# Kernel optimization log

Hardware: AMD Instinct MI355X
Metric: run time of the kernel (lower is better)

Reference implementation:

```python
import jax, jax.numpy as jnp
import numpy as np

B, T, N, H, P = 16, 64, 512, 128, 12


def _laplacian_with_self_loop(adj):
    a = adj + jnp.eye(adj.shape[0], dtype=adj.dtype)
    d_inv_sqrt = 1.0 / jnp.sqrt(a.sum(axis=1))
    return a * d_inv_sqrt[:, None] * d_inv_sqrt[None, :]


def setup_inputs() -> dict:
    key = jax.random.key(0)
    ks = jax.random.split(key, 10)
    inputs = jax.random.normal(ks[0], (B, T, N), dtype=jnp.float32)
    adj = jax.random.uniform(ks[1], (N, N), dtype=jnp.float32)
    adj = (adj + adj.T) * 0.5
    laplacian = _laplacian_with_self_loop(adj)

    def xavier(k, shape):
        fan_in, fan_out = shape[0], shape[1]
        lim = np.sqrt(6.0 / (fan_in + fan_out))
        return jax.random.uniform(k, shape, jnp.float32, -lim, lim)

    W1 = xavier(ks[2], (H + 1, 2 * H))      # graph_conv1 weights
    b1 = jnp.ones((2 * H,), jnp.float32)    # bias init 1.0
    W2 = xavier(ks[3], (H + 1, H))          # graph_conv2 weights
    b2 = jnp.zeros((H,), jnp.float32)
    att_w1 = xavier(ks[4], (H, 1))
    att_w2 = xavier(ks[5], (N, 1))
    att_w3 = xavier(ks[6], (N, 1))
    att_b1 = jnp.zeros((1,), jnp.float32)
    att_b2 = jnp.zeros((1,), jnp.float32)
    att_b3 = jnp.zeros((1,), jnp.float32)
    W_out = xavier(ks[7], (T, P))
    b_out = jnp.zeros((P,), jnp.float32)
    return dict(inputs=inputs, laplacian=laplacian, W1=W1, b1=b1, W2=W2, b2=b2,
                att_w1=att_w1, att_w2=att_w2, att_w3=att_w3,
                att_b1=att_b1, att_b2=att_b2, att_b3=att_b3,
                W_out=W_out, b_out=b_out)


def reference(inputs, laplacian, W1, b1, W2, b2,
              att_w1, att_w2, att_w3, att_b1, att_b2, att_b3,
              W_out, b_out):
    Bs, Ts, Ns = inputs.shape
    Hs = W2.shape[1]

    def graph_conv(x_t, h_flat, W, b):
        # x_t: [B,N]; h_flat: [B, N*H]
        h = h_flat.reshape(Bs, Ns, Hs)
        conc = jnp.concatenate([x_t[..., None], h], axis=-1)     # [B,N,H+1]
        agg = jnp.einsum('mn,bnc->bmc', laplacian, conc)          # [B,N,H+1]
        out = agg @ W + b                                         # [B,N,O]
        return out.reshape(Bs, -1)                                # [B,N*O] (flattened, matching torch)

    def step(h_flat, x_t):
        ru = jax.nn.sigmoid(graph_conv(x_t, h_flat, W1, b1))      # [B, N*2H]
        r, u = jnp.split(ru, 2, axis=1)                            # split on flattened dim (faithful)
        c = jnp.tanh(graph_conv(x_t, r * h_flat, W2, b2))          # [B, N*H]
        new_h = u * h_flat + (1.0 - u) * c
        return new_h, new_h

    h0 = jnp.zeros((Bs, Ns * Hs), inputs.dtype)
    _, hs = jax.lax.scan(step, h0, jnp.moveaxis(inputs, 1, 0))     # [T,B,N*H]
    hidden_states = jnp.moveaxis(hs, 0, 1).reshape(Bs, Ts, Ns, Hs)

    # SelfAttention: project H->1, then N->1 per (b,t), softmax over T
    hs1 = hidden_states.reshape(-1, Hs) @ att_w1 + att_b1          # [B*T*N, 1]
    f = (hs1.reshape(-1, Ns) @ att_w2 + att_b2).reshape(Bs, Ts)
    g = (hs1.reshape(-1, Ns) @ att_w3 + att_b3).reshape(Bs, Ts)
    beta = jax.nn.softmax(g * f, axis=-1)                          # [B,T]
    context = beta[:, :, None] * hs1.reshape(Bs, Ts, Ns)           # [B,T,N]

    context = context.transpose(0, 2, 1)                           # [B,N,T]
    Ps = W_out.shape[1]
    out = (context.reshape(-1, Ts) @ W_out + b_out).reshape(Bs, Ns, Ps)
    return out.transpose(0, 2, 1)                                  # [B,pre_len,N]
```

## Files before the change

kernel.cpp:

```cpp
#include <hip/hip_runtime.h>
#include <math.h>

#define B_ 16
#define T_ 64
#define N_ 512
#define H_ 128
#define P_ 12
#define NH 65536

__global__ __launch_bounds__(512) void lx_kernel(const float* __restrict__ x,
                                                 const float* __restrict__ L,
                                                 float* __restrict__ Lx) {
    __shared__ __align__(16) float xs[2][N_];
    const int r0 = blockIdx.x * 2;
    const int tid = threadIdx.x;
    for (int j = 0; j < 2; ++j)
        xs[j][tid] = x[(size_t)(r0 + j) * N_ + tid];
    __syncthreads();
    float a0 = 0.f, a1 = 0.f;
    const int m = tid;
#pragma unroll 8
    for (int n = 0; n < N_; ++n) {
        float lv = L[(size_t)n * N_ + m];
        a0 += xs[0][n] * lv;
        a1 += xs[1][n] * lv;
    }
    Lx[(size_t)(r0 + 0) * N_ + m] = a0;
    Lx[(size_t)(r0 + 1) * N_ + m] = a1;
}

#define FMA4(dst, a, hv)                                                      \
    dst[0] += (a) * (hv).x; dst[1] += (a) * (hv).y;                           \
    dst[2] += (a) * (hv).z; dst[3] += (a) * (hv).w;

__global__ __launch_bounds__(512) void gc1y_kernel(
    const float* __restrict__ L, const float* __restrict__ Hprev,
    const float* __restrict__ Lx, const float* __restrict__ W1,
    const float* __restrict__ b1, const float* __restrict__ W2,
    float* __restrict__ Y, float* __restrict__ u, int t) {
    __shared__ __align__(16) union Buf {
        float Ht[2][32][H_];
        struct { float R[32][132]; float Zb[16][132]; } s;
    } bb;
    __shared__ __align__(16) union LW {
        float Lt[2][32][20];
        float Wt[16][260];
    } sm;

    const int tid = threadIdx.x;
    const int b = blockIdx.x & 15;
    const int m0 = (blockIdx.x >> 4) * 16;
    const float* __restrict__ Hb = Hprev + (size_t)b * NH;

    const int hrow = tid >> 5, hcol = (tid & 31) * 4;
    const int lm = tid >> 5, lk = tid & 31;

    {
        *(float4*)&bb.Ht[0][hrow][hcol] =
            *(const float4*)&Hb[(size_t)hrow * H_ + hcol];
        *(float4*)&bb.Ht[0][hrow + 16][hcol] =
            *(const float4*)&Hb[(size_t)(hrow + 16) * H_ + hcol];
        sm.Lt[0][lk][lm] = L[(size_t)(m0 + lm) * N_ + lk];
    }
    __syncthreads();

    const int g = tid >> 6;
    const int l = tid & 63;
    const int ty = l >> 4;
    const int tx = l & 15;
    const int ma0 = ty * 4;
    const int ca0 = tx * 4, cb0 = 64 + tx * 4;

    float acc[4][2][4] = {};

    for (int kc = 0; kc < 16; ++kc) {
        const int bi = kc & 1, bj = bi ^ 1;
        float4 p0, p1;
        float pl;
        if (kc < 15) {
            const size_t kb = (size_t)(kc + 1) * 32;
            p0 = *(const float4*)&Hb[(kb + hrow) * H_ + hcol];
            p1 = *(const float4*)&Hb[(kb + hrow + 16) * H_ + hcol];
            pl = L[(size_t)(m0 + lm) * N_ + kb + lk];
        }
#pragma unroll
        for (int kk = 0; kk < 4; ++kk) {
            const int k = g * 4 + kk;
            const float4 la = *(const float4*)&sm.Lt[bi][k][ma0];
            const float4 h0 = *(const float4*)&bb.Ht[bi][k][ca0];
            const float4 h1 = *(const float4*)&bb.Ht[bi][k][cb0];
            FMA4(acc[0][0], la.x, h0) FMA4(acc[0][1], la.x, h1)
            FMA4(acc[1][0], la.y, h0) FMA4(acc[1][1], la.y, h1)
            FMA4(acc[2][0], la.z, h0) FMA4(acc[2][1], la.z, h1)
            FMA4(acc[3][0], la.w, h0) FMA4(acc[3][1], la.w, h1)
        }
        if (kc < 15) {
            *(float4*)&bb.Ht[bj][hrow][hcol] = p0;
            *(float4*)&bb.Ht[bj][hrow + 16][hcol] = p1;
            sm.Lt[bj][lk][lm] = pl;
        }
        __syncthreads();
    }

    for (int r = 0; r < 8; ++r) {
        if (g == r) {
#pragma unroll
            for (int i = 0; i < 4; ++i) {
#pragma unroll
                for (int v = 0; v < 2; ++v) {
                    const int c = v ? cb0 : ca0;
                    float4* zp = (float4*)&bb.s.Zb[ma0 + i][c];
                    if (r == 0) {
                        *zp = make_float4(acc[i][v][0], acc[i][v][1],
                                          acc[i][v][2], acc[i][v][3]);
                    } else {
                        float4 z = *zp;
                        *zp = make_float4(z.x + acc[i][v][0], z.y + acc[i][v][1],
                                          z.z + acc[i][v][2], z.w + acc[i][v][3]);
                    }
                }
            }
        }
        __syncthreads();
    }

    const int wv8 = tid >> 6;
    const int lr = l >> 3;
    const int lc = wv8 * 32 + (l & 7) * 4;
    float a2[2][4] = {};
    const int wr = tid >> 5, wc = (tid & 31) * 4;

#pragma unroll 1
    for (int ck = 0; ck < 8; ++ck) {
        *(float4*)&sm.Wt[wr][wc] =
            *(const float4*)&W1[(size_t)(1 + ck * 16 + wr) * 256 + wc];
        *(float4*)&sm.Wt[wr][wc + 128] =
            *(const float4*)&W1[(size_t)(1 + ck * 16 + wr) * 256 + wc + 128];
        __syncthreads();
#pragma unroll
        for (int ch4 = 0; ch4 < 4; ++ch4) {
            const int cc = ck * 16 + ch4 * 4;
            const float4 z0v = *(const float4*)&bb.s.Zb[lr][cc];
            const float4 z1v = *(const float4*)&bb.s.Zb[lr + 8][cc];
            const float4 w0v = *(const float4*)&sm.Wt[ch4 * 4 + 0][lc];
            const float4 w1v = *(const float4*)&sm.Wt[ch4 * 4 + 1][lc];
            const float4 w2v = *(const float4*)&sm.Wt[ch4 * 4 + 2][lc];
            const float4 w3v = *(const float4*)&sm.Wt[ch4 * 4 + 3][lc];
            a2[0][0] += z0v.x * w0v.x + z0v.y * w1v.x + z0v.z * w2v.x + z0v.w * w3v.x;
            a2[0][1] += z0v.x * w0v.y + z0v.y * w1v.y + z0v.z * w2v.y + z0v.w * w3v.y;
            a2[0][2] += z0v.x * w0v.z + z0v.y * w1v.z + z0v.z * w2v.z + z0v.w * w3v.z;
            a2[0][3] += z0v.x * w0v.w + z0v.y * w1v.w + z0v.z * w2v.w + z0v.w * w3v.w;
            a2[1][0] += z1v.x * w0v.x + z1v.y * w1v.x + z1v.z * w2v.x + z1v.w * w3v.x;
            a2[1][1] += z1v.x * w0v.y + z1v.y * w1v.y + z1v.z * w2v.y + z1v.w * w3v.y;
            a2[1][2] += z1v.x * w0v.z + z1v.y * w1v.z + z1v.z * w2v.z + z1v.w * w3v.z;
            a2[1][3] += z1v.x * w0v.w + z1v.y * w1v.w + z1v.z * w2v.w + z1v.w * w3v.w;
        }
        __syncthreads();
    }

    const float4 w0r = *(const float4*)&W1[lc];
    const float4 bbv = *(const float4*)&b1[lc];
    const float* __restrict__ LxRow = Lx + ((size_t)b * T_ + t) * N_ + m0;
    const bool isR = (m0 < 256);

    if (isR) {
#pragma unroll
        for (int i = 0; i < 2; ++i) {
            const int mi = lr + 8 * i;
            const float lx = LxRow[mi];
            float v0 = a2[i][0] + lx * w0r.x + bbv.x;
            float v1 = a2[i][1] + lx * w0r.y + bbv.y;
            float v2 = a2[i][2] + lx * w0r.z + bbv.z;
            float v3 = a2[i][3] + lx * w0r.w + bbv.w;
            float s0 = 1.f / (1.f + expf(-v0));
            float s1 = 1.f / (1.f + expf(-v1));
            float s2 = 1.f / (1.f + expf(-v2));
            float s3 = 1.f / (1.f + expf(-v3));
            const int fl = (m0 + mi) * 256 + lc;
            float4 hv = *(const float4*)&Hb[fl];
            *(float4*)&bb.s.R[2 * mi + (lc >> 7)][lc & 127] =
                make_float4(s0 * hv.x, s1 * hv.y, s2 * hv.z, s3 * hv.w);
        }
        __syncthreads();

        const int pr = l >> 2;
        const int pc = wv8 * 16 + (l & 3) * 4;
        float a3[2][4] = {};
#pragma unroll 1
        for (int ck = 0; ck < 8; ++ck) {
            *(float4*)&sm.Wt[wr][wc] =
                *(const float4*)&W2[(size_t)(1 + ck * 16 + wr) * H_ + wc];
            __syncthreads();
#pragma unroll
            for (int ch4 = 0; ch4 < 4; ++ch4) {
                const int cc = ck * 16 + ch4 * 4;
                const float4 z0v = *(const float4*)&bb.s.R[pr][cc];
                const float4 z1v = *(const float4*)&bb.s.R[pr + 16][cc];
                const float4 w0v = *(const float4*)&sm.Wt[ch4 * 4 + 0][pc];
                const float4 w1v = *(const float4*)&sm.Wt[ch4 * 4 + 1][pc];
                const float4 w2v = *(const float4*)&sm.Wt[ch4 * 4 + 2][pc];
                const float4 w3v = *(const float4*)&sm.Wt[ch4 * 4 + 3][pc];
                a3[0][0] += z0v.x * w0v.x + z0v.y * w1v.x + z0v.z * w2v.x + z0v.w * w3v.x;
                a3[0][1] += z0v.x * w0v.y + z0v.y * w1v.y + z0v.z * w2v.y + z0v.w * w3v.y;
                a3[0][2] += z0v.x * w0v.z + z0v.y * w1v.z + z0v.z * w2v.z + z0v.w * w3v.z;
                a3[0][3] += z0v.x * w0v.w + z0v.y * w1v.w + z0v.z * w2v.w + z0v.w * w3v.w;
                a3[1][0] += z1v.x * w0v.x + z1v.y * w1v.x + z1v.z * w2v.x + z1v.w * w3v.x;
                a3[1][1] += z1v.x * w0v.y + z1v.y * w1v.y + z1v.z * w2v.y + z1v.w * w3v.y;
                a3[1][2] += z1v.x * w0v.z + z1v.y * w1v.z + z1v.z * w2v.z + z1v.w * w3v.z;
                a3[1][3] += z1v.x * w0v.w + z1v.y * w1v.w + z1v.z * w2v.w + z1v.w * w3v.w;
            }
            __syncthreads();
        }
        float* __restrict__ Yb = Y + (size_t)b * NH;
        *(float4*)&Yb[(size_t)(2 * m0 + pr) * H_ + pc] =
            make_float4(a3[0][0], a3[0][1], a3[0][2], a3[0][3]);
        *(float4*)&Yb[(size_t)(2 * m0 + pr + 16) * H_ + pc] =
            make_float4(a3[1][0], a3[1][1], a3[1][2], a3[1][3]);
    } else {
        float* __restrict__ uB = u + (size_t)b * NH;
#pragma unroll
        for (int i = 0; i < 2; ++i) {
            const int mi = lr + 8 * i;
            const float lx = LxRow[mi];
            float v0 = a2[i][0] + lx * w0r.x + bbv.x;
            float v1 = a2[i][1] + lx * w0r.y + bbv.y;
            float v2 = a2[i][2] + lx * w0r.z + bbv.z;
            float v3 = a2[i][3] + lx * w0r.w + bbv.w;
            float s0 = 1.f / (1.f + expf(-v0));
            float s1 = 1.f / (1.f + expf(-v1));
            float s2 = 1.f / (1.f + expf(-v2));
            float s3 = 1.f / (1.f + expf(-v3));
            const int fl = (m0 + mi) * 256 + lc;
            *(float4*)&uB[fl - NH] = make_float4(s0, s1, s2, s3);
        }
    }
}

__global__ __launch_bounds__(512) void gcz_kernel(
    const float* __restrict__ L, const float* __restrict__ Y,
    const float* __restrict__ Hprev, const float* __restrict__ u,
    const float* __restrict__ Lx, const float* __restrict__ W2,
    const float* __restrict__ b2, const float* __restrict__ aw1,
    const float* __restrict__ ab1, float* __restrict__ Hnew,
    float* __restrict__ hs1, int t) {
    __shared__ __align__(16) union Buf {
        float Ht[2][32][H_];
        struct { float R[32][H_]; float Zb[16][H_]; } s;
    } bb;
    __shared__ __align__(16) float Lt[2][32][20];

    const int tid = threadIdx.x;
    const int b = blockIdx.x & 15;
    const int m0 = (blockIdx.x >> 4) * 16;
    const float* __restrict__ Yb = Y + (size_t)b * NH;

    const int hrow = tid >> 5, hcol = (tid & 31) * 4;
    const int lm = tid >> 5, lk = tid & 31;

    {
        *(float4*)&bb.Ht[0][hrow][hcol] =
            *(const float4*)&Yb[(size_t)hrow * H_ + hcol];
        *(float4*)&bb.Ht[0][hrow + 16][hcol] =
            *(const float4*)&Yb[(size_t)(hrow + 16) * H_ + hcol];
        Lt[0][lk][lm] = L[(size_t)(m0 + lm) * N_ + lk];
    }
    __syncthreads();

    const int g = tid >> 6;
    const int l = tid & 63;
    const int ty = l >> 4;
    const int tx = l & 15;
    const int ma0 = ty * 4;
    const int ca0 = tx * 4, cb0 = 64 + tx * 4;

    float acc[4][2][4] = {};

    for (int kc = 0; kc < 16; ++kc) {
        const int bi = kc & 1, bj = bi ^ 1;
        float4 p0, p1;
        float pl;
        if (kc < 15) {
            const size_t kb = (size_t)(kc + 1) * 32;
            p0 = *(const float4*)&Yb[(kb + hrow) * H_ + hcol];
            p1 = *(const float4*)&Yb[(kb + hrow + 16) * H_ + hcol];
            pl = L[(size_t)(m0 + lm) * N_ + kb + lk];
        }
#pragma unroll
        for (int kk = 0; kk < 4; ++kk) {
            const int k = g * 4 + kk;
            const float4 la = *(const float4*)&Lt[bi][k][ma0];
            const float4 h0 = *(const float4*)&bb.Ht[bi][k][ca0];
            const float4 h1 = *(const float4*)&bb.Ht[bi][k][cb0];
            FMA4(acc[0][0], la.x, h0) FMA4(acc[0][1], la.x, h1)
            FMA4(acc[1][0], la.y, h0) FMA4(acc[1][1], la.y, h1)
            FMA4(acc[2][0], la.z, h0) FMA4(acc[2][1], la.z, h1)
            FMA4(acc[3][0], la.w, h0) FMA4(acc[3][1], la.w, h1)
        }
        if (kc < 15) {
            *(float4*)&bb.Ht[bj][hrow][hcol] = p0;
            *(float4*)&bb.Ht[bj][hrow + 16][hcol] = p1;
            Lt[bj][lk][lm] = pl;
        }
        __syncthreads();
    }

    for (int r = 0; r < 8; ++r) {
        if (g == r) {
#pragma unroll
            for (int i = 0; i < 4; ++i) {
#pragma unroll
                for (int v = 0; v < 2; ++v) {
                    const int c = v ? cb0 : ca0;
                    float4* zp = (float4*)&bb.s.Zb[ma0 + i][c];
                    if (r == 0) {
                        *zp = make_float4(acc[i][v][0], acc[i][v][1],
                                          acc[i][v][2], acc[i][v][3]);
                    } else {
                        float4 z = *zp;
                        *zp = make_float4(z.x + acc[i][v][0], z.y + acc[i][v][1],
                                          z.z + acc[i][v][2], z.w + acc[i][v][3]);
                    }
                }
            }
        }
        __syncthreads();
    }

    const int zr = tid >> 5;
    const int zc = (tid & 31) * 4;
    const float4 zv = *(const float4*)&bb.s.Zb[zr][zc];
    const float4 w0r = *(const float4*)&W2[zc];
    const float4 bbv = *(const float4*)&b2[zc];
    const float4 awv = *(const float4*)&aw1[zc];
    const float lx = Lx[((size_t)b * T_ + t) * N_ + m0 + zr];

    float c0 = tanhf(zv.x + lx * w0r.x + bbv.x);
    float c1 = tanhf(zv.y + lx * w0r.y + bbv.y);
    float c2 = tanhf(zv.z + lx * w0r.z + bbv.z);
    float c3 = tanhf(zv.w + lx * w0r.w + bbv.w);

    const size_t fl = (size_t)b * NH + (size_t)(m0 + zr) * H_ + zc;
    const float4 uv = *(const float4*)&u[fl];
    const float4 hp = *(const float4*)&Hprev[fl];
    const float h0 = uv.x * hp.x + (1.f - uv.x) * c0;
    const float h1 = uv.y * hp.y + (1.f - uv.y) * c1;
    const float h2 = uv.z * hp.z + (1.f - uv.z) * c2;
    const float h3 = uv.w * hp.w + (1.f - uv.w) * c3;
    *(float4*)&Hnew[fl] = make_float4(h0, h1, h2, h3);

    float part = h0 * awv.x + h1 * awv.y + h2 * awv.z + h3 * awv.w;
#pragma unroll
    for (int off = 16; off; off >>= 1) part += __shfl_xor(part, off);
    if ((tid & 31) == 0)
        hs1[((size_t)b * T_ + t) * N_ + m0 + zr] = part + ab1[0];
}

__global__ __launch_bounds__(64) void att_beta_kernel(
    const float* __restrict__ hs1, const float* __restrict__ aw2,
    const float* __restrict__ aw3, const float* __restrict__ ab2,
    const float* __restrict__ ab3, float* __restrict__ beta) {
    const int b = blockIdx.x;
    const int t = threadIdx.x;
    const float* __restrict__ row = hs1 + ((size_t)b * T_ + t) * N_;
    float f = 0.f, g = 0.f;
    for (int n = 0; n < N_; n += 4) {
        float4 hv = *(const float4*)&row[n];
        float4 w2v = *(const float4*)&aw2[n];
        float4 w3v = *(const float4*)&aw3[n];
        f += hv.x * w2v.x + hv.y * w2v.y + hv.z * w2v.z + hv.w * w2v.w;
        g += hv.x * w3v.x + hv.y * w3v.y + hv.z * w3v.z + hv.w * w3v.w;
    }
    f += ab2[0];
    g += ab3[0];
    float s = f * g;
    float mx = s;
    for (int off = 32; off; off >>= 1) mx = fmaxf(mx, __shfl_xor(mx, off));
    float e = expf(s - mx);
    float sum = e;
    for (int off = 32; off; off >>= 1) sum += __shfl_xor(sum, off);
    beta[b * T_ + t] = e / sum;
}

__global__ __launch_bounds__(256) void att_out_kernel(
    const float* __restrict__ hs1, const float* __restrict__ beta,
    const float* __restrict__ Wout, const float* __restrict__ bout,
    float* __restrict__ out) {
    __shared__ float bs[T_];
    __shared__ float ws[T_][P_];
    const int b = blockIdx.x;
    const int tid = threadIdx.x;
    if (tid < T_) bs[tid] = beta[b * T_ + tid];
    for (int i = tid; i < T_ * P_; i += 256) ws[i / P_][i % P_] = Wout[i];
    __syncthreads();
    for (int nn = 0; nn < 2; ++nn) {
        const int n = tid + nn * 256;
        float acc[P_];
#pragma unroll
        for (int p = 0; p < P_; ++p) acc[p] = bout[p];
        for (int t = 0; t < T_; ++t) {
            float v = bs[t] * hs1[((size_t)b * T_ + t) * N_ + n];
#pragma unroll
            for (int p = 0; p < P_; ++p) acc[p] += v * ws[t][p];
        }
#pragma unroll
        for (int p = 0; p < P_; ++p) out[((size_t)b * P_ + p) * N_ + n] = acc[p];
    }
}

extern "C" void kernel_launch(void* const* d_in, const int* in_sizes, int n_in,
                              void* d_out, int out_size, void* d_ws, size_t ws_size,
                              hipStream_t stream) {
    const float* x = (const float*)d_in[0];
    const float* L = (const float*)d_in[1];
    const float* W1 = (const float*)d_in[2];
    const float* b1 = (const float*)d_in[3];
    const float* W2 = (const float*)d_in[4];
    const float* b2 = (const float*)d_in[5];
    const float* aw1 = (const float*)d_in[6];
    const float* aw2 = (const float*)d_in[7];
    const float* aw3 = (const float*)d_in[8];
    const float* ab1 = (const float*)d_in[9];
    const float* ab2 = (const float*)d_in[10];
    const float* ab3 = (const float*)d_in[11];
    const float* Wout = (const float*)d_in[12];
    const float* bout = (const float*)d_in[13];
    float* out = (float*)d_out;

    float* ws = (float*)d_ws;
    float* Lx = ws;
    float* hs1 = Lx + B_ * T_ * N_;
    float* hb0 = hs1 + B_ * T_ * N_;
    float* hb1 = hb0 + (size_t)B_ * NH;
    float* u = hb1 + (size_t)B_ * NH;
    float* Ybuf = u + (size_t)B_ * NH;
    float* beta = Ybuf + (size_t)B_ * NH;
    (void)in_sizes; (void)n_in; (void)out_size; (void)ws_size;

    hipMemsetAsync(hb0, 0, (size_t)B_ * NH * sizeof(float), stream);
    lx_kernel<<<512, 512, 0, stream>>>(x, L, Lx);

    for (int t = 0; t < T_; ++t) {
        float* hp = (t & 1) ? hb1 : hb0;
        float* hn = (t & 1) ? hb0 : hb1;
        gc1y_kernel<<<512, 512, 0, stream>>>(L, hp, Lx, W1, b1, W2, Ybuf, u, t);
        gcz_kernel<<<512, 512, 0, stream>>>(L, Ybuf, hp, u, Lx, W2, b2, aw1,
                                            ab1, hn, hs1, t);
    }
    att_beta_kernel<<<16, 64, 0, stream>>>(hs1, aw2, aw3, ab2, ab3, beta);
    att_out_kernel<<<16, 256, 0, stream>>>(hs1, beta, Wout, bout, out);
}
```

Baseline: 3.583 ms.

## Stage full L slice in LDS and read H and W directly from global

```diff
diff --git a/kernel.cpp b/kernel.cpp
--- a/kernel.cpp
+++ b/kernel.cpp
@@ -39,29 +39,20 @@
     const float* __restrict__ b1, const float* __restrict__ W2,
     float* __restrict__ Y, float* __restrict__ u, int t) {
     __shared__ __align__(16) union Buf {
-        float Ht[2][32][H_];
+        float Lt[512][20];
         struct { float R[32][132]; float Zb[16][132]; } s;
     } bb;
-    __shared__ __align__(16) union LW {
-        float Lt[2][32][20];
-        float Wt[16][260];
-    } sm;
 
     const int tid = threadIdx.x;
     const int b = blockIdx.x & 15;
     const int m0 = (blockIdx.x >> 4) * 16;
     const float* __restrict__ Hb = Hprev + (size_t)b * NH;
 
-    const int hrow = tid >> 5, hcol = (tid & 31) * 4;
     const int lm = tid >> 5, lk = tid & 31;
 
-    {
-        *(float4*)&bb.Ht[0][hrow][hcol] =
-            *(const float4*)&Hb[(size_t)hrow * H_ + hcol];
-        *(float4*)&bb.Ht[0][hrow + 16][hcol] =
-            *(const float4*)&Hb[(size_t)(hrow + 16) * H_ + hcol];
-        sm.Lt[0][lk][lm] = L[(size_t)(m0 + lm) * N_ + lk];
-    }
+#pragma unroll
+    for (int j = 0; j < 16; ++j)
+        bb.Lt[lk + 32 * j][lm] = L[(size_t)(m0 + lm) * N_ + lk + 32 * j];
     __syncthreads();
 
     const int g = tid >> 6;
@@ -72,35 +63,24 @@
     const int ca0 = tx * 4, cb0 = 64 + tx * 4;
 
     float acc[4][2][4] = {};
-
+    const float* __restrict__ h0p = Hb + ca0;
+    const float* __restrict__ h1p = Hb + cb0;
+
+#pragma unroll 1
     for (int kc = 0; kc < 16; ++kc) {
-        const int bi = kc & 1, bj = bi ^ 1;
-        float4 p0, p1;
-        float pl;
-        if (kc < 15) {
-            const size_t kb = (size_t)(kc + 1) * 32;
-            p0 = *(const float4*)&Hb[(kb + hrow) * H_ + hcol];
-            p1 = *(const float4*)&Hb[(kb + hrow + 16) * H_ + hcol];
-            pl = L[(size_t)(m0 + lm) * N_ + kb + lk];
-        }
 #pragma unroll
         for (int kk = 0; kk < 4; ++kk) {
-            const int k = g * 4 + kk;
-            const float4 la = *(const float4*)&sm.Lt[bi][k][ma0];
-            const float4 h0 = *(const float4*)&bb.Ht[bi][k][ca0];
-            const float4 h1 = *(const float4*)&bb.Ht[bi][k][cb0];
+            const int k = kc * 32 + g * 4 + kk;
+            const float4 la = *(const float4*)&bb.Lt[k][ma0];
+            const float4 h0 = *(const float4*)&h0p[(size_t)k * H_];
+            const float4 h1 = *(const float4*)&h1p[(size_t)k * H_];
             FMA4(acc[0][0], la.x, h0) FMA4(acc[0][1], la.x, h1)
             FMA4(acc[1][0], la.y, h0) FMA4(acc[1][1], la.y, h1)
             FMA4(acc[2][0], la.z, h0) FMA4(acc[2][1], la.z, h1)
             FMA4(acc[3][0], la.w, h0) FMA4(acc[3][1], la.w, h1)
         }
-        if (kc < 15) {
-            *(float4*)&bb.Ht[bj][hrow][hcol] = p0;
-            *(float4*)&bb.Ht[bj][hrow + 16][hcol] = p1;
-            sm.Lt[bj][lk][lm] = pl;
-        }
-        __syncthreads();
-    }
+    }
+    __syncthreads();
 
     for (int r = 0; r < 8; ++r) {
         if (g == r) {
@@ -128,24 +108,19 @@
     const int lr = l >> 3;
     const int lc = wv8 * 32 + (l & 7) * 4;
     float a2[2][4] = {};
-    const int wr = tid >> 5, wc = (tid & 31) * 4;
 
 #pragma unroll 1
     for (int ck = 0; ck < 8; ++ck) {
-        *(float4*)&sm.Wt[wr][wc] =
-            *(const float4*)&W1[(size_t)(1 + ck * 16 + wr) * 256 + wc];
-        *(float4*)&sm.Wt[wr][wc + 128] =
-            *(const float4*)&W1[(size_t)(1 + ck * 16 + wr) * 256 + wc + 128];
-        __syncthreads();
 #pragma unroll
         for (int ch4 = 0; ch4 < 4; ++ch4) {
             const int cc = ck * 16 + ch4 * 4;
             const float4 z0v = *(const float4*)&bb.s.Zb[lr][cc];
             const float4 z1v = *(const float4*)&bb.s.Zb[lr + 8][cc];
-            const float4 w0v = *(const float4*)&sm.Wt[ch4 * 4 + 0][lc];
-            const float4 w1v = *(const float4*)&sm.Wt[ch4 * 4 + 1][lc];
-            const float4 w2v = *(const float4*)&sm.Wt[ch4 * 4 + 2][lc];
-            const float4 w3v = *(const float4*)&sm.Wt[ch4 * 4 + 3][lc];
+            const int wrow = 1 + ck * 16 + ch4 * 4;
+            const float4 w0v = *(const float4*)&W1[(size_t)(wrow + 0) * 256 + lc];
+            const float4 w1v = *(const float4*)&W1[(size_t)(wrow + 1) * 256 + lc];
+            const float4 w2v = *(const float4*)&W1[(size_t)(wrow + 2) * 256 + lc];
+            const float4 w3v = *(const float4*)&W1[(size_t)(wrow + 3) * 256 + lc];
             a2[0][0] += z0v.x * w0v.x + z0v.y * w1v.x + z0v.z * w2v.x + z0v.w * w3v.x;
             a2[0][1] += z0v.x * w0v.y + z0v.y * w1v.y + z0v.z * w2v.y + z0v.w * w3v.y;
             a2[0][2] += z0v.x * w0v.z + z0v.y * w1v.z + z0v.z * w2v.z + z0v.w * w3v.z;
@@ -155,7 +130,6 @@
             a2[1][2] += z1v.x * w0v.z + z1v.y * w1v.z + z1v.z * w2v.z + z1v.w * w3v.z;
             a2[1][3] += z1v.x * w0v.w + z1v.y * w1v.w + z1v.z * w2v.w + z1v.w * w3v.w;
         }
-        __syncthreads();
     }
 
     const float4 w0r = *(const float4*)&W1[lc];
@@ -188,28 +162,25 @@
         float a3[2][4] = {};
 #pragma unroll 1
         for (int ck = 0; ck < 8; ++ck) {
-            *(float4*)&sm.Wt[wr][wc] =
-                *(const float4*)&W2[(size_t)(1 + ck * 16 + wr) * H_ + wc];
-            __syncthreads();
 #pragma unroll
             for (int ch4 = 0; ch4 < 4; ++ch4) {
                 const int cc = ck * 16 + ch4 * 4;
-                const float4 z0v = *(const float4*)&bb.s.R[pr][cc];
-                const float4 z1v = *(const float4*)&bb.s.R[pr + 16][cc];
-                const float4 w0v = *(const float4*)&sm.Wt[ch4 * 4 + 0][pc];
-                const float4 w1v = *(const float4*)&sm.Wt[ch4 * 4 + 1][pc];
-                const float4 w2v = *(const float4*)&sm.Wt[ch4 * 4 + 2][pc];
-                const float4 w3v = *(const float4*)&sm.Wt[ch4 * 4 + 3][pc];
-                a3[0][0] += z0v.x * w0v.x + z0v.y * w1v.x + z0v.z * w2v.x + z0v.w * w3v.x;
-                a3[0][1] += z0v.x * w0v.y + z0v.y * w1v.y + z0v.z * w2v.y + z0v.w * w3v.y;
-                a3[0][2] += z0v.x * w0v.z + z0v.y * w1v.z + z0v.z * w2v.z + z0v.w * w3v.z;
-                a3[0][3] += z0v.x * w0v.w + z0v.y * w1v.w + z0v.z * w2v.w + z0v.w * w3v.w;
-                a3[1][0] += z1v.x * w0v.x + z1v.y * w1v.x + z1v.z * w2v.x + z1v.w * w3v.x;
-                a3[1][1] += z1v.x * w0v.y + z1v.y * w1v.y + z1v.z * w2v.y + z1v.w * w3v.y;
-                a3[1][2] += z1v.x * w0v.z + z1v.y * w1v.z + z1v.z * w2v.z + z1v.w * w3v.z;
-                a3[1][3] += z1v.x * w0v.w + z1v.y * w1v.w + z1v.z * w2v.w + z1v.w * w3v.w;
+                const float4 z0 = *(const float4*)&bb.s.R[pr][cc];
+                const float4 z1 = *(const float4*)&bb.s.R[pr + 16][cc];
+                const int wrow = 1 + ck * 16 + ch4 * 4;
+                const float4 w0 = *(const float4*)&W2[(size_t)(wrow + 0) * H_ + pc];
+                const float4 w1 = *(const float4*)&W2[(size_t)(wrow + 1) * H_ + pc];
+                const float4 w2 = *(const float4*)&W2[(size_t)(wrow + 2) * H_ + pc];
+                const float4 w3 = *(const float4*)&W2[(size_t)(wrow + 3) * H_ + pc];
+                a3[0][0] += z0.x * w0.x + z0.y * w1.x + z0.z * w2.x + z0.w * w3.x;
+                a3[0][1] += z0.x * w0.y + z0.y * w1.y + z0.z * w2.y + z0.w * w3.y;
+                a3[0][2] += z0.x * w0.z + z0.y * w1.z + z0.z * w2.z + z0.w * w3.z;
+                a3[0][3] += z0.x * w0.w + z0.y * w1.w + z0.z * w2.w + z0.w * w3.w;
+                a3[1][0] += z1.x * w0.x + z1.y * w1.x + z1.z * w2.x + z1.w * w3.x;
+                a3[1][1] += z1.x * w0.y + z1.y * w1.y + z1.z * w2.y + z1.w * w3.y;
+                a3[1][2] += z1.x * w0.z + z1.y * w1.z + z1.z * w2.z + z1.w * w3.z;
+                a3[1][3] += z1.x * w0.w + z1.y * w1.w + z1.z * w2.w + z1.w * w3.w;
             }
-            __syncthreads();
         }
         float* __restrict__ Yb = Y + (size_t)b * NH;
         *(float4*)&Yb[(size_t)(2 * m0 + pr) * H_ + pc] =
@@ -244,26 +215,19 @@
     const float* __restrict__ ab1, float* __restrict__ Hnew,
     float* __restrict__ hs1, int t) {
     __shared__ __align__(16) union Buf {
-        float Ht[2][32][H_];
-        struct { float R[32][H_]; float Zb[16][H_]; } s;
+        float Lt[512][20];
+        float Zb[16][H_];
     } bb;
-    __shared__ __align__(16) float Lt[2][32][20];
 
     const int tid = threadIdx.x;
     const int b = blockIdx.x & 15;
     const int m0 = (blockIdx.x >> 4) * 16;
     const float* __restrict__ Yb = Y + (size_t)b * NH;
 
-    const int hrow = tid >> 5, hcol = (tid & 31) * 4;
     const int lm = tid >> 5, lk = tid & 31;
-
-    {
-        *(float4*)&bb.Ht[0][hrow][hcol] =
-            *(const float4*)&Yb[(size_t)hrow * H_ + hcol];
-        *(float4*)&bb.Ht[0][hrow + 16][hcol] =
-            *(const float4*)&Yb[(size_t)(hrow + 16) * H_ + hcol];
-        Lt[0][lk][lm] = L[(size_t)(m0 + lm) * N_ + lk];
-    }
+#pragma unroll
+    for (int j = 0; j < 16; ++j)
+        bb.Lt[lk + 32 * j][lm] = L[(size_t)(m0 + lm) * N_ + lk + 32 * j];
     __syncthreads();
 
     const int g = tid >> 6;
@@ -274,35 +238,24 @@
     const int ca0 = tx * 4, cb0 = 64 + tx * 4;
 
     float acc[4][2][4] = {};
-
+    const float* __restrict__ y0p = Yb + ca0;
+    const float* __restrict__ y1p = Yb + cb0;
+
+#pragma unroll 1
     for (int kc = 0; kc < 16; ++kc) {
-        const int bi = kc & 1, bj = bi ^ 1;
-        float4 p0, p1;
-        float pl;
-        if (kc < 15) {
-            const size_t kb = (size_t)(kc + 1) * 32;
-            p0 = *(const float4*)&Yb[(kb + hrow) * H_ + hcol];
-            p1 = *(const float4*)&Yb[(kb + hrow + 16) * H_ + hcol];
-            pl = L[(size_t)(m0 + lm) * N_ + kb + lk];
-        }
 #pragma unroll
         for (int kk = 0; kk < 4; ++kk) {
-            const int k = g * 4 + kk;
-            const float4 la = *(const float4*)&Lt[bi][k][ma0];
-            const float4 h0 = *(const float4*)&bb.Ht[bi][k][ca0];
-            const float4 h1 = *(const float4*)&bb.Ht[bi][k][cb0];
+            const int k = kc * 32 + g * 4 + kk;
+            const float4 la = *(const float4*)&bb.Lt[k][ma0];
+            const float4 h0 = *(const float4*)&y0p[(size_t)k * H_];
+            const float4 h1 = *(const float4*)&y1p[(size_t)k * H_];
             FMA4(acc[0][0], la.x, h0) FMA4(acc[0][1], la.x, h1)
             FMA4(acc[1][0], la.y, h0) FMA4(acc[1][1], la.y, h1)
             FMA4(acc[2][0], la.z, h0) FMA4(acc[2][1], la.z, h1)
             FMA4(acc[3][0], la.w, h0) FMA4(acc[3][1], la.w, h1)
         }
-        if (kc < 15) {
-            *(float4*)&bb.Ht[bj][hrow][hcol] = p0;
-            *(float4*)&bb.Ht[bj][hrow + 16][hcol] = p1;
-            Lt[bj][lk][lm] = pl;
-        }
-        __syncthreads();
-    }
+    }
+    __syncthreads();
 
     for (int r = 0; r < 8; ++r) {
         if (g == r) {
@@ -311,7 +264,7 @@
 #pragma unroll
                 for (int v = 0; v < 2; ++v) {
                     const int c = v ? cb0 : ca0;
-                    float4* zp = (float4*)&bb.s.Zb[ma0 + i][c];
+                    float4* zp = (float4*)&bb.Zb[ma0 + i][c];
                     if (r == 0) {
                         *zp = make_float4(acc[i][v][0], acc[i][v][1],
                                           acc[i][v][2], acc[i][v][3]);
@@ -328,7 +281,7 @@
 
     const int zr = tid >> 5;
     const int zc = (tid & 31) * 4;
-    const float4 zv = *(const float4*)&bb.s.Zb[zr][zc];
+    const float4 zv = *(const float4*)&bb.Zb[zr][zc];
     const float4 w0r = *(const float4*)&W2[zc];
     const float4 bbv = *(const float4*)&b2[zc];
     const float4 awv = *(const float4*)&aw1[zc];
```

After: 4.187 ms. 1.17x slower.

## Halve gc1y row tile to 8 rows and double grid to 1024 blocks

Applied to the files above, without the earlier changes.

```diff
diff --git a/kernel.cpp b/kernel.cpp
--- a/kernel.cpp
+++ b/kernel.cpp
@@ -33,34 +33,38 @@
     dst[0] += (a) * (hv).x; dst[1] += (a) * (hv).y;                           \
     dst[2] += (a) * (hv).z; dst[3] += (a) * (hv).w;
 
-__global__ __launch_bounds__(512) void gc1y_kernel(
+__global__ __launch_bounds__(512, 8) void gc1y_kernel(
     const float* __restrict__ L, const float* __restrict__ Hprev,
     const float* __restrict__ Lx, const float* __restrict__ W1,
     const float* __restrict__ b1, const float* __restrict__ W2,
     float* __restrict__ Y, float* __restrict__ u, int t) {
     __shared__ __align__(16) union Buf {
         float Ht[2][32][H_];
-        struct { float R[32][132]; float Zb[16][132]; } s;
+        struct {
+            float R[16][132];
+            float Zb[8][132];
+            float Wt[16][260];
+        } s;
     } bb;
-    __shared__ __align__(16) union LW {
-        float Lt[2][32][20];
-        float Wt[16][260];
-    } sm;
+    __shared__ __align__(16) float Lt[2][32][14];
 
     const int tid = threadIdx.x;
     const int b = blockIdx.x & 15;
-    const int m0 = (blockIdx.x >> 4) * 16;
+    const int mt = blockIdx.x >> 4;
+    const bool isR = (mt & 1) == 0;
+    const int m0 = (mt >> 1) * 8 + (isR ? 0 : 256);
     const float* __restrict__ Hb = Hprev + (size_t)b * NH;
 
     const int hrow = tid >> 5, hcol = (tid & 31) * 4;
-    const int lm = tid >> 5, lk = tid & 31;
 
     {
         *(float4*)&bb.Ht[0][hrow][hcol] =
             *(const float4*)&Hb[(size_t)hrow * H_ + hcol];
         *(float4*)&bb.Ht[0][hrow + 16][hcol] =
             *(const float4*)&Hb[(size_t)(hrow + 16) * H_ + hcol];
-        sm.Lt[0][lk][lm] = L[(size_t)(m0 + lm) * N_ + lk];
+        if (tid < 256)
+            Lt[0][tid & 31][tid >> 5] =
+                L[(size_t)(m0 + (tid >> 5)) * N_ + (tid & 31)];
     }
     __syncthreads();
 
@@ -68,10 +72,10 @@
     const int l = tid & 63;
     const int ty = l >> 4;
     const int tx = l & 15;
-    const int ma0 = ty * 4;
+    const int ma0 = ty * 2;
     const int ca0 = tx * 4, cb0 = 64 + tx * 4;
 
-    float acc[4][2][4] = {};
+    float acc[2][2][4] = {};
 
     for (int kc = 0; kc < 16; ++kc) {
         const int bi = kc & 1, bj = bi ^ 1;
@@ -81,23 +85,23 @@
             const size_t kb = (size_t)(kc + 1) * 32;
             p0 = *(const float4*)&Hb[(kb + hrow) * H_ + hcol];
             p1 = *(const float4*)&Hb[(kb + hrow + 16) * H_ + hcol];
-            pl = L[(size_t)(m0 + lm) * N_ + kb + lk];
+            if (tid < 256)
+                pl = L[(size_t)(m0 + (tid >> 5)) * N_ + kb + (tid & 31)];
         }
 #pragma unroll
         for (int kk = 0; kk < 4; ++kk) {
             const int k = g * 4 + kk;
-            const float4 la = *(const float4*)&sm.Lt[bi][k][ma0];
+            const float2 la = *(const float2*)&Lt[bi][k][ma0];
             const float4 h0 = *(const float4*)&bb.Ht[bi][k][ca0];
             const float4 h1 = *(const float4*)&bb.Ht[bi][k][cb0];
             FMA4(acc[0][0], la.x, h0) FMA4(acc[0][1], la.x, h1)
             FMA4(acc[1][0], la.y, h0) FMA4(acc[1][1], la.y, h1)
-            FMA4(acc[2][0], la.z, h0) FMA4(acc[2][1], la.z, h1)
-            FMA4(acc[3][0], la.w, h0) FMA4(acc[3][1], la.w, h1)
         }
         if (kc < 15) {
             *(float4*)&bb.Ht[bj][hrow][hcol] = p0;
             *(float4*)&bb.Ht[bj][hrow + 16][hcol] = p1;
-            sm.Lt[bj][lk][lm] = pl;
+            if (tid < 256)
+                Lt[bj][tid & 31][tid >> 5] = pl;
         }
         __syncthreads();
     }
@@ -105,7 +109,7 @@
     for (int r = 0; r < 8; ++r) {
         if (g == r) {
 #pragma unroll
-            for (int i = 0; i < 4; ++i) {
+            for (int i = 0; i < 2; ++i) {
 #pragma unroll
                 for (int v = 0; v < 2; ++v) {
                     const int c = v ? cb0 : ca0;
@@ -127,112 +131,82 @@
     const int wv8 = tid >> 6;
     const int lr = l >> 3;
     const int lc = wv8 * 32 + (l & 7) * 4;
-    float a2[2][4] = {};
     const int wr = tid >> 5, wc = (tid & 31) * 4;
+    float a2[4] = {};
 
 #pragma unroll 1
     for (int ck = 0; ck < 8; ++ck) {
-        *(float4*)&sm.Wt[wr][wc] =
+        *(float4*)&bb.s.Wt[wr][wc] =
             *(const float4*)&W1[(size_t)(1 + ck * 16 + wr) * 256 + wc];
-        *(float4*)&sm.Wt[wr][wc + 128] =
+        *(float4*)&bb.s.Wt[wr][wc + 128] =
             *(const float4*)&W1[(size_t)(1 + ck * 16 + wr) * 256 + wc + 128];
         __syncthreads();
 #pragma unroll
         for (int ch4 = 0; ch4 < 4; ++ch4) {
             const int cc = ck * 16 + ch4 * 4;
-            const float4 z0v = *(const float4*)&bb.s.Zb[lr][cc];
-            const float4 z1v = *(const float4*)&bb.s.Zb[lr + 8][cc];
-            const float4 w0v = *(const float4*)&sm.Wt[ch4 * 4 + 0][lc];
-            const float4 w1v = *(const float4*)&sm.Wt[ch4 * 4 + 1][lc];
-            const float4 w2v = *(const float4*)&sm.Wt[ch4 * 4 + 2][lc];
-            const float4 w3v = *(const float4*)&sm.Wt[ch4 * 4 + 3][lc];
-            a2[0][0] += z0v.x * w0v.x + z0v.y * w1v.x + z0v.z * w2v.x + z0v.w * w3v.x;
-            a2[0][1] += z0v.x * w0v.y + z0v.y * w1v.y + z0v.z * w2v.y + z0v.w * w3v.y;
-            a2[0][2] += z0v.x * w0v.z + z0v.y * w1v.z + z0v.z * w2v.z + z0v.w * w3v.z;
-            a2[0][3] += z0v.x * w0v.w + z0v.y * w1v.w + z0v.z * w2v.w + z0v.w * w3v.w;
-            a2[1][0] += z1v.x * w0v.x + z1v.y * w1v.x + z1v.z * w2v.x + z1v.w * w3v.x;
-            a2[1][1] += z1v.x * w0v.y + z1v.y * w1v.y + z1v.z * w2v.y + z1v.w * w3v.y;
-            a2[1][2] += z1v.x * w0v.z + z1v.y * w1v.z + z1v.z * w2v.z + z1v.w * w3v.z;
-            a2[1][3] += z1v.x * w0v.w + z1v.y * w1v.w + z1v.z * w2v.w + z1v.w * w3v.w;
+            const float4 zv = *(const float4*)&bb.s.Zb[lr][cc];
+            const float4 w0v = *(const float4*)&bb.s.Wt[ch4 * 4 + 0][lc];
+            const float4 w1v = *(const float4*)&bb.s.Wt[ch4 * 4 + 1][lc];
+            const float4 w2v = *(const float4*)&bb.s.Wt[ch4 * 4 + 2][lc];
+            const float4 w3v = *(const float4*)&bb.s.Wt[ch4 * 4 + 3][lc];
+            a2[0] += zv.x * w0v.x + zv.y * w1v.x + zv.z * w2v.x + zv.w * w3v.x;
+            a2[1] += zv.x * w0v.y + zv.y * w1v.y + zv.z * w2v.y + zv.w * w3v.y;
+            a2[2] += zv.x * w0v.z + zv.y * w1v.z + zv.z * w2v.z + zv.w * w3v.z;
+            a2[3] += zv.x * w0v.w + zv.y * w1v.w + zv.z * w2v.w + zv.w * w3v.w;
         }
         __syncthreads();
     }
 
     const float4 w0r = *(const float4*)&W1[lc];
     const float4 bbv = *(const float4*)&b1[lc];
-    const float* __restrict__ LxRow = Lx + ((size_t)b * T_ + t) * N_ + m0;
-    const bool isR = (m0 < 256);
+    const float lx = Lx[((size_t)b * T_ + t) * N_ + m0 + lr];
+
+    float v0 = a2[0] + lx * w0r.x + bbv.x;
+    float v1 = a2[1] + lx * w0r.y + bbv.y;
+    float v2 = a2[2] + lx * w0r.z + bbv.z;
+    float v3 = a2[3] + lx * w0r.w + bbv.w;
+    float s0 = 1.f / (1.f + expf(-v0));
+    float s1 = 1.f / (1.f + expf(-v1));
+    float s2 = 1.f / (1.f + expf(-v2));
+    float s3 = 1.f / (1.f + expf(-v3));
 
     if (isR) {
-#pragma unroll
-        for (int i = 0; i < 2; ++i) {
-            const int mi = lr + 8 * i;
-            const float lx = LxRow[mi];
-            float v0 = a2[i][0] + lx * w0r.x + bbv.x;
-            float v1 = a2[i][1] + lx * w0r.y + bbv.y;
-            float v2 = a2[i][2] + lx * w0r.z + bbv.z;
-            float v3 = a2[i][3] + lx * w0r.w + bbv.w;
-            float s0 = 1.f / (1.f + expf(-v0));
-            float s1 = 1.f / (1.f + expf(-v1));
-            float s2 = 1.f / (1.f + expf(-v2));
-            float s3 = 1.f / (1.f + expf(-v3));
-            const int fl = (m0 + mi) * 256 + lc;
-            float4 hv = *(const float4*)&Hb[fl];
-            *(float4*)&bb.s.R[2 * mi + (lc >> 7)][lc & 127] =
-                make_float4(s0 * hv.x, s1 * hv.y, s2 * hv.z, s3 * hv.w);
-        }
+        const int fl = (m0 + lr) * 256 + lc;
+        const float4 hv = *(const float4*)&Hb[fl];
+        *(float4*)&bb.s.R[2 * lr + (lc >> 7)][lc & 127] =
+            make_float4(s0 * hv.x, s1 * hv.y, s2 * hv.z, s3 * hv.w);
         __syncthreads();
 
         const int pr = l >> 2;
         const int pc = wv8 * 16 + (l & 3) * 4;
-        float a3[2][4] = {};
+        float a3[4] = {};
 #pragma unroll 1
         for (int ck = 0; ck < 8; ++ck) {
-            *(float4*)&sm.Wt[wr][wc] =
+            *(float4*)&bb.s.Wt[wr][wc] =
                 *(const float4*)&W2[(size_t)(1 + ck * 16 + wr) * H_ + wc];
             __syncthreads();
 #pragma unroll
             for (int ch4 = 0; ch4 < 4; ++ch4) {
                 const int cc = ck * 16 + ch4 * 4;
-                const float4 z0v = *(const float4*)&bb.s.R[pr][cc];
-                const float4 z1v = *(const float4*)&bb.s.R[pr + 16][cc];
-                const float4 w0v = *(const float4*)&sm.Wt[ch4 * 4 + 0][pc];
-                const float4 w1v = *(const float4*)&sm.Wt[ch4 * 4 + 1][pc];
-                const float4 w2v = *(const float4*)&sm.Wt[ch4 * 4 + 2][pc];
-                const float4 w3v = *(const float4*)&sm.Wt[ch4 * 4 + 3][pc];
-                a3[0][0] += z0v.x * w0v.x + z0v.y * w1v.x + z0v.z * w2v.x + z0v.w * w3v.x;
-                a3[0][1] += z0v.x * w0v.y + z0v.y * w1v.y + z0v.z * w2v.y + z0v.w * w3v.y;
-                a3[0][2] += z0v.x * w0v.z + z0v.y * w1v.z + z0v.z * w2v.z + z0v.w * w3v.z;
-                a3[0][3] += z0v.x * w0v.w + z0v.y * w1v.w + z0v.z * w2v.w + z0v.w * w3v.w;
-                a3[1][0] += z1v.x * w0v.x + z1v.y * w1v.x + z1v.z * w2v.x + z1v.w * w3v.x;
-                a3[1][1] += z1v.x * w0v.y + z1v.y * w1v.y + z1v.z * w2v.y + z1v.w * w3v.y;
-                a3[1][2] += z1v.x * w0v.z + z1v.y * w1v.z + z1v.z * w2v.z + z1v.w * w3v.z;
-                a3[1][3] += z1v.x * w0v.w + z1v.y * w1v.w + z1v.z * w2v.w + z1v.w * w3v.w;
+                const float4 z0 = *(const float4*)&bb.s.R[pr][cc];
+                const float4 w0 = *(const float4*)&bb.s.Wt[ch4 * 4 + 0][pc];
+                const float4 w1 = *(const float4*)&bb.s.Wt[ch4 * 4 + 1][pc];
+                const float4 w2 = *(const float4*)&bb.s.Wt[ch4 * 4 + 2][pc];
+                const float4 w3 = *(const float4*)&bb.s.Wt[ch4 * 4 + 3][pc];
+                a3[0] += z0.x * w0.x + z0.y * w1.x + z0.z * w2.x + z0.w * w3.x;
+                a3[1] += z0.x * w0.y + z0.y * w1.y + z0.z * w2.y + z0.w * w3.y;
+                a3[2] += z0.x * w0.z + z0.y * w1.z + z0.z * w2.z + z0.w * w3.z;
+                a3[3] += z0.x * w0.w + z0.y * w1.w + z0.z * w2.w + z0.w * w3.w;
             }
             __syncthreads();
         }
         float* __restrict__ Yb = Y + (size_t)b * NH;
         *(float4*)&Yb[(size_t)(2 * m0 + pr) * H_ + pc] =
-            make_float4(a3[0][0], a3[0][1], a3[0][2], a3[0][3]);
-        *(float4*)&Yb[(size_t)(2 * m0 + pr + 16) * H_ + pc] =
-            make_float4(a3[1][0], a3[1][1], a3[1][2], a3[1][3]);
+            make_float4(a3[0], a3[1], a3[2], a3[3]);
     } else {
         float* __restrict__ uB = u + (size_t)b * NH;
-#pragma unroll
-        for (int i = 0; i < 2; ++i) {
-            const int mi = lr + 8 * i;
-            const float lx = LxRow[mi];
-            float v0 = a2[i][0] + lx * w0r.x + bbv.x;
-            float v1 = a2[i][1] + lx * w0r.y + bbv.y;
-            float v2 = a2[i][2] + lx * w0r.z + bbv.z;
-            float v3 = a2[i][3] + lx * w0r.w + bbv.w;
-            float s0 = 1.f / (1.f + expf(-v0));
-            float s1 = 1.f / (1.f + expf(-v1));
-            float s2 = 1.f / (1.f + expf(-v2));
-            float s3 = 1.f / (1.f + expf(-v3));
-            const int fl = (m0 + mi) * 256 + lc;
-            *(float4*)&uB[fl - NH] = make_float4(s0, s1, s2, s3);
-        }
+        const int fl = (m0 + lr - 256) * 256 + lc;
+        *(float4*)&uB[fl] = make_float4(s0, s1, s2, s3);
     }
 }
 
@@ -442,7 +416,7 @@
     for (int t = 0; t < T_; ++t) {
         float* hp = (t & 1) ? hb1 : hb0;
         float* hn = (t & 1) ? hb0 : hb1;
-        gc1y_kernel<<<512, 512, 0, stream>>>(L, hp, Lx, W1, b1, W2, Ybuf, u, t);
+        gc1y_kernel<<<1024, 512, 0, stream>>>(L, hp, Lx, W1, b1, W2, Ybuf, u, t);
         gcz_kernel<<<512, 512, 0, stream>>>(L, Ybuf, hp, u, Lx, W2, b2, aw1,
                                             ab1, hn, hs1, t);
     }
```

After: 6.896 ms. +92.5%, slower.
